# Kernel optimization log

Measured on AMD Instinct MI355X. Metric: run time of the kernel, lower is better.

Reference implementation:

```python
import jax, jax.numpy as jnp
import numpy as np

IN_F = 4096
OUT_F = 4096
Q_LEVELS = 16  # 4-bit


def setup_inputs() -> dict:
    key = jax.random.key(0)
    k = jax.random.split(key, 7)
    input = jax.random.normal(k[0], (4, 128, IN_F), dtype=jnp.float32)
    qweight = jax.random.randint(k[1], (OUT_F, IN_F), 0, Q_LEVELS, dtype=jnp.int32)
    scales = jax.random.uniform(k[2], (OUT_F, 1), dtype=jnp.float32)
    zeros = jax.random.uniform(k[3], (OUT_F, 1), dtype=jnp.float32)
    outlier = jax.random.uniform(k[4], (OUT_F, IN_F), dtype=jnp.float32)
    grad_updates = jax.random.normal(k[5], (OUT_F, IN_F), dtype=jnp.float32)
    bias = jax.random.normal(k[6], (OUT_F,), dtype=jnp.float32)
    return {"input": input, "qweight": qweight, "scales": scales,
            "zeros": zeros, "outlier": outlier,
            "grad_updates": grad_updates, "bias": bias}


def reference(input, qweight, scales, zeros, outlier, grad_updates, bias):
    # dequantize: affine per-output-row quantization -> dense weight [out, in]
    weight = (qweight.astype(jnp.float32) - zeros) * scales
    # sparse outlier correction (densified), scaled by learned GradUpdates
    weight = weight + outlier * grad_updates
    # F.linear: y = x @ W^T + b
    return jnp.einsum('bsi,oi->bso', input, weight) + bias
```

## Files before the change

### kernel.cpp

```cpp
#include <hip/hip_runtime.h>
#include <stdint.h>

#define IN_F   4096
#define OUT_F  4096
#define M_TOT  512
#define KT     (IN_F / 32)
#define BN     32
#define BK     64
#define KSPLIT 2
#define KPB    (IN_F / KSPLIT)
#define NITER  (KPB / BK)
#define NBUF   16

typedef unsigned short u16;
typedef __bf16 bf16x8 __attribute__((ext_vector_type(8)));
typedef float  f32x4  __attribute__((ext_vector_type(4)));

__device__ __forceinline__ u16 f2bf(float x) {
    unsigned u = __float_as_uint(x);
    u += 0x7FFFu + ((u >> 16) & 1u);
    return (u16)(u >> 16);
}

__global__ void pack_a_kernel(const float* __restrict__ in, u16* __restrict__ aws) {
    int t    = blockIdx.x * blockDim.x + threadIdx.x;
    int lane = t & 63;
    int kt   = (t >> 6) & (KT - 1);
    int mt   = t >> 13;
    int m = mt * 16 + (lane & 15);
    int k = kt * 32 + ((lane >> 4) << 3);
    const float* src = in + (size_t)m * IN_F + k;
    float4 a0 = *(const float4*)src;
    float4 a1 = *(const float4*)(src + 4);
    union { u16 u[8]; uint4 v; } pk;
    pk.u[0]=f2bf(a0.x); pk.u[1]=f2bf(a0.y); pk.u[2]=f2bf(a0.z); pk.u[3]=f2bf(a0.w);
    pk.u[4]=f2bf(a1.x); pk.u[5]=f2bf(a1.y); pk.u[6]=f2bf(a1.z); pk.u[7]=f2bf(a1.w);
    *(uint4*)(aws + (size_t)t * 8) = pk.v;
}

__global__ __launch_bounds__(1024, 4) void qlinear_kernel(
    const u16*   __restrict__ aws,
    const int*   __restrict__ qw,
    const float* __restrict__ scales,
    const float* __restrict__ zeros,
    const float* __restrict__ outlier,
    const float* __restrict__ grad,
    float*       __restrict__ part)
{
    __shared__ __align__(16) u16 Bsh[NBUF][4 * 64 * 8];
    __shared__ unsigned ready[NBUF];
    __shared__ unsigned freed[NBUF];

    const int tid  = threadIdx.x;
    const int lane = tid & 63;
    const int wv   = tid >> 6;

    if (tid < NBUF) { ready[tid] = 0; freed[tid] = 0; }
    __syncthreads();

    const int nblk  = blockIdx.x >> 1;
    const int khalf = blockIdx.x & 1;
    const int n0    = nblk * BN;
    const int k0    = khalf * KPB;

    if (wv >= 8) {
        const int pt   = tid - 512;
        const int row  = pt >> 4;
        const int kc4  = (pt & 15) * 4;
        const int orow = n0 + row;
        const float sr = scales[orow];
        const float c0 = -zeros[orow] * sr;
        const size_t g0 = (size_t)orow * IN_F + k0 + kc4;

        const int j0    = kc4 & 7;
        const int frag  = ((kc4 >> 5) << 1) + (row >> 4);
        const int flane = (row & 15) | (((kc4 >> 3) & 3) << 4);
        const int doff  = (frag * 64 + flane) * 8 + j0;

        int4 qb[2]; float4 ob[2], gb[2];
        auto ld = [&](int r, int s) {
            size_t off = g0 + (size_t)r * BK;
            qb[s] = *(const int4*)  (qw      + off);
            ob[s] = *(const float4*)(outlier + off);
            gb[s] = *(const float4*)(grad    + off);
        };
        ld(0, 0);
        ld(1, 1);

        #pragma unroll 2
        for (int r = 0; r < NITER; ++r) {
            int b = r & (NBUF - 1);
            if (r >= NBUF) {
                unsigned need = 8u * (unsigned)(r / NBUF);
                while (__hip_atomic_load(&freed[b], __ATOMIC_ACQUIRE,
                                         __HIP_MEMORY_SCOPE_WORKGROUP) < need)
                    __builtin_amdgcn_s_sleep(1);
            }
            int s = r & 1;
            union { u16 u[4]; uint2 v; } pk;
            pk.u[0] = f2bf(fmaf((float)qb[s].x, sr, fmaf(ob[s].x, gb[s].x, c0)));
            pk.u[1] = f2bf(fmaf((float)qb[s].y, sr, fmaf(ob[s].y, gb[s].y, c0)));
            pk.u[2] = f2bf(fmaf((float)qb[s].z, sr, fmaf(ob[s].z, gb[s].z, c0)));
            pk.u[3] = f2bf(fmaf((float)qb[s].w, sr, fmaf(ob[s].w, gb[s].w, c0)));
            *(uint2*)(&Bsh[b][doff]) = pk.v;
            if (lane == 0)
                __hip_atomic_fetch_add(&ready[b], 1u, __ATOMIC_RELEASE,
                                       __HIP_MEMORY_SCOPE_WORKGROUP);
            if (r + 2 < NITER) ld(r + 2, s);
        }
    } else {
        const int cw = wv;
        const u16* abase = aws + ((size_t)(cw * 4) * KT + (size_t)khalf * (KPB / 32)) * 512
                               + (size_t)lane * 8;
        f32x4 acc[4][2] = {};

        #pragma unroll 1
        for (int r = 0; r < NITER; ++r) {
            int b = r & (NBUF - 1);
            unsigned need = 8u * (unsigned)(r / NBUF + 1);
            while (__hip_atomic_load(&ready[b], __ATOMIC_ACQUIRE,
                                     __HIP_MEMORY_SCOPE_WORKGROUP) < need)
                __builtin_amdgcn_s_sleep(1);

            const u16* bb = &Bsh[b][0];
            bf16x8 bfr[2][2], af[2][4];
            #pragma unroll
            for (int ks = 0; ks < 2; ++ks)
                #pragma unroll
                for (int nf = 0; nf < 2; ++nf)
                    bfr[ks][nf] = *(const bf16x8*)(bb + ((ks * 2 + nf) * 64 + lane) * 8);
            #pragma unroll
            for (int ks = 0; ks < 2; ++ks)
                #pragma unroll
                for (int mf = 0; mf < 4; ++mf)
                    af[ks][mf] = *(const bf16x8*)(abase + ((size_t)mf * KT + r * 2 + ks) * 512);
            #pragma unroll
            for (int ks = 0; ks < 2; ++ks)
                #pragma unroll
                for (int mf = 0; mf < 4; ++mf)
                    #pragma unroll
                    for (int nf = 0; nf < 2; ++nf)
                        acc[mf][nf] = __builtin_amdgcn_mfma_f32_16x16x32_bf16(
                            af[ks][mf], bfr[ks][nf], acc[mf][nf], 0, 0, 0);

            if (lane == 0)
                __hip_atomic_fetch_add(&freed[b], 1u, __ATOMIC_RELEASE,
                                       __HIP_MEMORY_SCOPE_WORKGROUP);
        }

        float* pout = part + (size_t)khalf * (M_TOT * OUT_F);
        const int cm0 = cw * 64 + ((lane >> 4) << 2);
        const int cn0 = n0 + (lane & 15);
        #pragma unroll
        for (int mf = 0; mf < 4; ++mf)
            #pragma unroll
            for (int nf = 0; nf < 2; ++nf) {
                float* op = pout + (size_t)(cm0 + mf * 16) * OUT_F + cn0 + nf * 16;
                #pragma unroll
                for (int rr = 0; rr < 4; ++rr)
                    op[(size_t)rr * OUT_F] = acc[mf][nf][rr];
            }
    }
}

__global__ void reduce_kernel(const float4* __restrict__ part,
                              const float4* __restrict__ bias,
                              float4* __restrict__ out) {
    int idx = blockIdx.x * blockDim.x + threadIdx.x;
    float4 s = bias[idx & (OUT_F / 4 - 1)];
    const int STRIDE = M_TOT * OUT_F / 4;
    #pragma unroll
    for (int k = 0; k < KSPLIT; ++k) {
        float4 p = part[(size_t)k * STRIDE + idx];
        s.x += p.x; s.y += p.y; s.z += p.z; s.w += p.w;
    }
    out[idx] = s;
}

extern "C" void kernel_launch(void* const* d_in, const int* in_sizes, int n_in,
                              void* d_out, int out_size, void* d_ws, size_t ws_size,
                              hipStream_t stream) {
    const float* input   = (const float*)d_in[0];
    const int*   qweight = (const int*)  d_in[1];
    const float* scales  = (const float*)d_in[2];
    const float* zeros   = (const float*)d_in[3];
    const float* outlier = (const float*)d_in[4];
    const float* grad    = (const float*)d_in[5];
    const float* bias    = (const float*)d_in[6];
    float* out = (float*)d_out;

    u16*   aws  = (u16*)d_ws;
    float* part = (float*)((char*)d_ws + (4u << 20));

    pack_a_kernel<<<(M_TOT * IN_F / 8) / 256, 256, 0, stream>>>(input, aws);
    qlinear_kernel<<<(OUT_F / BN) * KSPLIT, 1024, 0, stream>>>(
        aws, qweight, scales, zeros, outlier, grad, part);
    reduce_kernel<<<(M_TOT * OUT_F / 4) / 256, 256, 0, stream>>>(
        (const float4*)part, (const float4*)bias, (float4*)out);
}
```

Baseline: 269.7 us.

## Replace warp-specialized producer/consumer pipeline with uniform double-buffered blocks

Drops the split into producer and consumer waves that synchronized through shared-memory atomic flags over a 16-stage ring. Every wave now both dequantizes a slice of the weight tile into a two-stage shared buffer and runs MFMAs, with one __syncthreads per iteration. The tile becomes 16 output columns by 128 k, giving twice as many 512-thread blocks. This removes spin-wait overhead and idle specialized waves, but the A-fragment global loads are now repeated across twice as many N-blocks, and the barrier serializes the dequantize step with the compute.

```diff
diff --git a/kernel.cpp b/kernel.cpp
--- a/kernel.cpp
+++ b/kernel.cpp
@@ -5,12 +5,11 @@
 #define OUT_F  4096
 #define M_TOT  512
 #define KT     (IN_F / 32)
-#define BN     32
-#define BK     64
+#define BN     16
+#define BK     128
 #define KSPLIT 2
 #define KPB    (IN_F / KSPLIT)
 #define NITER  (KPB / BK)
-#define NBUF   16
 
 typedef unsigned short u16;
 typedef __bf16 bf16x8 __attribute__((ext_vector_type(8)));
@@ -38,7 +37,7 @@
     *(uint4*)(aws + (size_t)t * 8) = pk.v;
 }
 
-__global__ __launch_bounds__(1024, 4) void qlinear_kernel(
+__global__ __launch_bounds__(512, 4) void qlinear_kernel(
     const u16*   __restrict__ aws,
     const int*   __restrict__ qw,
     const float* __restrict__ scales,
@@ -47,119 +46,86 @@
     const float* __restrict__ grad,
     float*       __restrict__ part)
 {
-    __shared__ __align__(16) u16 Bsh[NBUF][4 * 64 * 8];
-    __shared__ unsigned ready[NBUF];
-    __shared__ unsigned freed[NBUF];
+    __shared__ __align__(16) u16 Bsh[2][4 * 64 * 8];
 
     const int tid  = threadIdx.x;
     const int lane = tid & 63;
     const int wv   = tid >> 6;
-
-    if (tid < NBUF) { ready[tid] = 0; freed[tid] = 0; }
-    __syncthreads();
 
     const int nblk  = blockIdx.x >> 1;
     const int khalf = blockIdx.x & 1;
     const int n0    = nblk * BN;
     const int k0    = khalf * KPB;
 
-    if (wv >= 8) {
-        const int pt   = tid - 512;
-        const int row  = pt >> 4;
-        const int kc4  = (pt & 15) * 4;
-        const int orow = n0 + row;
-        const float sr = scales[orow];
-        const float c0 = -zeros[orow] * sr;
-        const size_t g0 = (size_t)orow * IN_F + k0 + kc4;
+    const int srow = tid >> 5;
+    const int schk = tid & 31;
+    const int orow = n0 + srow;
+    const float sr = scales[orow];
+    const float c0 = -zeros[orow] * sr;
+    const size_t sg = (size_t)orow * IN_F + k0 + schk * 4;
+    const int sks   = schk >> 3;
+    const int squad = (schk >> 1) & 3;
+    const int j0    = (schk & 1) * 4;
+    const int slane = srow | (squad << 4);
+    const int doff  = (sks * 64 + slane) * 8 + j0;
 
-        const int j0    = kc4 & 7;
-        const int frag  = ((kc4 >> 5) << 1) + (row >> 4);
-        const int flane = (row & 15) | (((kc4 >> 3) & 3) << 4);
-        const int doff  = (frag * 64 + flane) * 8 + j0;
+    int4 qb[2]; float4 ob[2], gb[2];
+    auto ld = [&](int it) {
+        int s = it & 1;
+        size_t off = sg + (size_t)it * BK;
+        qb[s] = *(const int4*)  (qw      + off);
+        ob[s] = *(const float4*)(outlier + off);
+        gb[s] = *(const float4*)(grad    + off);
+    };
+    auto st = [&](int it) {
+        int s = it & 1;
+        union { u16 u[4]; uint2 v; } pk;
+        pk.u[0] = f2bf(fmaf((float)qb[s].x, sr, fmaf(ob[s].x, gb[s].x, c0)));
+        pk.u[1] = f2bf(fmaf((float)qb[s].y, sr, fmaf(ob[s].y, gb[s].y, c0)));
+        pk.u[2] = f2bf(fmaf((float)qb[s].z, sr, fmaf(ob[s].z, gb[s].z, c0)));
+        pk.u[3] = f2bf(fmaf((float)qb[s].w, sr, fmaf(ob[s].w, gb[s].w, c0)));
+        *(uint2*)(&Bsh[it & 1][doff]) = pk.v;
+    };
 
-        int4 qb[2]; float4 ob[2], gb[2];
-        auto ld = [&](int r, int s) {
-            size_t off = g0 + (size_t)r * BK;
-            qb[s] = *(const int4*)  (qw      + off);
-            ob[s] = *(const float4*)(outlier + off);
-            gb[s] = *(const float4*)(grad    + off);
-        };
-        ld(0, 0);
-        ld(1, 1);
+    const u16* abase = aws + ((size_t)(wv * 4) * KT + khalf * (KPB / 32)) * 512
+                           + (size_t)lane * 8;
 
-        #pragma unroll 2
-        for (int r = 0; r < NITER; ++r) {
-            int b = r & (NBUF - 1);
-            if (r >= NBUF) {
-                unsigned need = 8u * (unsigned)(r / NBUF);
-                while (__hip_atomic_load(&freed[b], __ATOMIC_ACQUIRE,
-                                         __HIP_MEMORY_SCOPE_WORKGROUP) < need)
-                    __builtin_amdgcn_s_sleep(1);
+    f32x4 acc[4] = {};
+
+    ld(0);
+    st(0);
+    ld(1);
+    __syncthreads();
+
+    for (int it = 0; it < NITER; ++it) {
+        const u16* bb = &Bsh[it & 1][0];
+        bf16x8 bfr[4];
+        #pragma unroll
+        for (int ks = 0; ks < 4; ++ks)
+            bfr[ks] = *(const bf16x8*)(bb + (ks * 64 + lane) * 8);
+
+        #pragma unroll
+        for (int ks = 0; ks < 4; ++ks) {
+            #pragma unroll
+            for (int mf = 0; mf < 4; ++mf) {
+                bf16x8 af = *(const bf16x8*)(abase + ((size_t)mf * KT + it * 4 + ks) * 512);
+                acc[mf] = __builtin_amdgcn_mfma_f32_16x16x32_bf16(af, bfr[ks], acc[mf], 0, 0, 0);
             }
-            int s = r & 1;
-            union { u16 u[4]; uint2 v; } pk;
-            pk.u[0] = f2bf(fmaf((float)qb[s].x, sr, fmaf(ob[s].x, gb[s].x, c0)));
-            pk.u[1] = f2bf(fmaf((float)qb[s].y, sr, fmaf(ob[s].y, gb[s].y, c0)));
-            pk.u[2] = f2bf(fmaf((float)qb[s].z, sr, fmaf(ob[s].z, gb[s].z, c0)));
-            pk.u[3] = f2bf(fmaf((float)qb[s].w, sr, fmaf(ob[s].w, gb[s].w, c0)));
-            *(uint2*)(&Bsh[b][doff]) = pk.v;
-            if (lane == 0)
-                __hip_atomic_fetch_add(&ready[b], 1u, __ATOMIC_RELEASE,
-                                       __HIP_MEMORY_SCOPE_WORKGROUP);
-            if (r + 2 < NITER) ld(r + 2, s);
-        }
-    } else {
-        const int cw = wv;
-        const u16* abase = aws + ((size_t)(cw * 4) * KT + (size_t)khalf * (KPB / 32)) * 512
-                               + (size_t)lane * 8;
-        f32x4 acc[4][2] = {};
-
-        #pragma unroll 1
-        for (int r = 0; r < NITER; ++r) {
-            int b = r & (NBUF - 1);
-            unsigned need = 8u * (unsigned)(r / NBUF + 1);
-            while (__hip_atomic_load(&ready[b], __ATOMIC_ACQUIRE,
-                                     __HIP_MEMORY_SCOPE_WORKGROUP) < need)
-                __builtin_amdgcn_s_sleep(1);
-
-            const u16* bb = &Bsh[b][0];
-            bf16x8 bfr[2][2], af[2][4];
-            #pragma unroll
-            for (int ks = 0; ks < 2; ++ks)
-                #pragma unroll
-                for (int nf = 0; nf < 2; ++nf)
-                    bfr[ks][nf] = *(const bf16x8*)(bb + ((ks * 2 + nf) * 64 + lane) * 8);
-            #pragma unroll
-            for (int ks = 0; ks < 2; ++ks)
-                #pragma unroll
-                for (int mf = 0; mf < 4; ++mf)
-                    af[ks][mf] = *(const bf16x8*)(abase + ((size_t)mf * KT + r * 2 + ks) * 512);
-            #pragma unroll
-            for (int ks = 0; ks < 2; ++ks)
-                #pragma unroll
-                for (int mf = 0; mf < 4; ++mf)
-                    #pragma unroll
-                    for (int nf = 0; nf < 2; ++nf)
-                        acc[mf][nf] = __builtin_amdgcn_mfma_f32_16x16x32_bf16(
-                            af[ks][mf], bfr[ks][nf], acc[mf][nf], 0, 0, 0);
-
-            if (lane == 0)
-                __hip_atomic_fetch_add(&freed[b], 1u, __ATOMIC_RELEASE,
-                                       __HIP_MEMORY_SCOPE_WORKGROUP);
         }
 
-        float* pout = part + (size_t)khalf * (M_TOT * OUT_F);
-        const int cm0 = cw * 64 + ((lane >> 4) << 2);
-        const int cn0 = n0 + (lane & 15);
+        if (it + 1 < NITER) st(it + 1);
+        if (it + 2 < NITER) ld(it + 2);
+        __syncthreads();
+    }
+
+    float* pout = part + (size_t)khalf * (M_TOT * OUT_F);
+    const int cm0 = wv * 64 + ((lane >> 4) << 2);
+    const int cn  = n0 + (lane & 15);
+    #pragma unroll
+    for (int mf = 0; mf < 4; ++mf) {
         #pragma unroll
-        for (int mf = 0; mf < 4; ++mf)
-            #pragma unroll
-            for (int nf = 0; nf < 2; ++nf) {
-                float* op = pout + (size_t)(cm0 + mf * 16) * OUT_F + cn0 + nf * 16;
-                #pragma unroll
-                for (int rr = 0; rr < 4; ++rr)
-                    op[(size_t)rr * OUT_F] = acc[mf][nf][rr];
-            }
+        for (int r = 0; r < 4; ++r)
+            pout[(size_t)(cm0 + mf * 16 + r) * OUT_F + cn] = acc[mf][r];
     }
 }
 
@@ -193,7 +159,7 @@
     float* part = (float*)((char*)d_ws + (4u << 20));
 
     pack_a_kernel<<<(M_TOT * IN_F / 8) / 256, 256, 0, stream>>>(input, aws);
-    qlinear_kernel<<<(OUT_F / BN) * KSPLIT, 1024, 0, stream>>>(
+    qlinear_kernel<<<(OUT_F / BN) * KSPLIT, 512, 0, stream>>>(
         aws, qweight, scales, zeros, outlier, grad, part);
     reduce_kernel<<<(M_TOT * OUT_F / 4) / 256, 256, 0, stream>>>(
         (const float4*)part, (const float4*)bias, (float4*)out);
```

Result: faster. 235.1 us (-12.8%).
